# Kernel tuning notes

Measured on AMD Instinct MI355X. Metric: run time of the kernel, lower is better.

The kernel has to match this reference:

```python
import jax, jax.numpy as jnp
from jax import lax
import numpy as np

N, M, P, K = 2, 16384, 5023, 4
C_PLANE, HP = 32, 256
OUT_DIM = 32


def _harmonic(x):
    # pytorch3d HarmonicEmbedding(n=4, logspace, omega_0=1, append_input=True)
    f = jnp.asarray([1.0, 2.0, 4.0, 8.0], x.dtype)
    e = (x[..., None] * f).reshape(x.shape[:-1] + (-1,))  # [..., 12]
    return jnp.concatenate([jnp.sin(e), jnp.cos(e), x], axis=-1)  # [..., 27]


def _grid_sample2d(img, grid):
    # img [C,H,W], grid [M,2] (x->W, y->H) in [-1,1]; bilinear, zero pad, align_corners=False
    C, H, W = img.shape
    x = (grid[:, 0] + 1.0) * (W / 2.0) - 0.5
    y = (grid[:, 1] + 1.0) * (H / 2.0) - 0.5
    x0 = jnp.floor(x); y0 = jnp.floor(y)
    x1 = x0 + 1.0; y1 = y0 + 1.0
    wx1 = x - x0; wx0 = 1.0 - wx1
    wy1 = y - y0; wy0 = 1.0 - wy1
    def gather(ix, iy):
        valid = ((ix >= 0) & (ix < W) & (iy >= 0) & (iy < H)).astype(img.dtype)
        ixc = jnp.clip(ix, 0, W - 1).astype(jnp.int32)
        iyc = jnp.clip(iy, 0, H - 1).astype(jnp.int32)
        return img[:, iyc, ixc] * valid[None, :]  # [C,M]
    out = (gather(x0, y0) * (wx0 * wy0) + gather(x1, y0) * (wx1 * wy0)
           + gather(x0, y1) * (wx0 * wy1) + gather(x1, y1) * (wx1 * wy1))
    return out.T  # [M,C]


def _forward(coordinates, directions, points_position, tex_tplanes, emb_table,
             pw1, pb1, pw2, pb2, fw1, fb1, fw2, fb2, fw3, fb3, dw, db, rw1, rb1, rw2, rb2):
    c = coordinates
    p = points_position
    # --- triplane sampling (EG3D projections (x,y),(x,z),(z,x)), mean over planes ---
    proj = jnp.stack([c[..., :2],
                      c[..., jnp.array([0, 2])],
                      c[..., jnp.array([2, 0])]], axis=1)  # [N,3,M,2]
    tex = jax.vmap(jax.vmap(_grid_sample2d))(tex_tplanes, proj).mean(axis=1)  # [N,M,32]
    # --- KNN (squared distances, ascending, as pytorch3d knn_points) ---
    d2 = (jnp.sum(c * c, -1)[:, :, None] + jnp.sum(p * p, -1)[:, None, :]
          - 2.0 * jnp.einsum('nmc,npc->nmp', c, p))  # [N,M,P]
    negd, idx = lax.top_k(-d2, K)
    dist = -negd  # [N,M,K]
    nn = jax.vmap(lambda pts, i: pts[i])(p, idx)  # [N,M,K,3]
    pf = emb_table[idx]  # [N,M,K,32]
    rel = c[:, :, None, :] - nn
    rel = rel / jnp.maximum(jnp.linalg.norm(rel, axis=-1, keepdims=True), 1e-12)
    h = jnp.concatenate([pf, _harmonic(rel)], axis=-1)  # [N,M,K,59]
    h = jax.nn.relu(h @ pw1 + pb1) @ pw2 + pb2  # [N,M,K,32]
    w = 1.0 / dist
    w = w / jnp.sum(w, axis=1, keepdims=True)  # dim=1 exactly as in source
    pts_feat = jnp.sum(h * w[..., None], axis=2)  # [N,M,32]
    # --- dense MLP stack ---
    feat = jnp.concatenate([tex, pts_feat], axis=-1)  # [N,M,64]
    feat = jax.nn.relu(feat @ fw1 + fb1)
    feat = jax.nn.relu(feat @ fw2 + fb2)
    feat = feat @ fw3 + fb3  # [N,M,128]
    selector = jnp.all((c > -1.0) & (c < 1.0), axis=-1)  # [N,M]
    raw = (jax.nn.softplus(10.0 * (feat @ dw + db)) / 10.0) * selector[..., None]
    densities = 1.0 - jnp.exp(-raw)
    rays = directions / jnp.maximum(jnp.linalg.norm(directions, axis=-1, keepdims=True), 1e-12)
    rgb = jnp.concatenate([feat, _harmonic(rays)], axis=-1)  # [N,M,155]
    rgb = jax.nn.relu(rgb @ rw1 + rb1) @ rw2 + rb2  # [N,M,OUT_DIM]
    rgb = jnp.concatenate([jax.nn.sigmoid(rgb[..., :3]) * (1.0 + 2 * 0.001) - 0.001,
                           rgb[..., 3:]], axis=-1)
    return densities, rgb, dist


def setup_inputs() -> dict:
    key = jax.random.key(0)
    ks = jax.random.split(key, 16)
    rn = lambda k, s, sc=1.0: jax.random.normal(k, s, jnp.float32) * sc
    def lin(k, i, o):
        k1, k2 = jax.random.split(k)
        return rn(k1, (i, o), 1.0 / np.sqrt(i)), rn(k2, (o,), 0.01)
    coordinates = jax.random.uniform(ks[0], (N, M, 3), jnp.float32)
    directions = rn(ks[1], (N, M, 3))
    points_position = jax.random.uniform(ks[2], (N, P, 3), jnp.float32)
    tex_tplanes = rn(ks[3], (N, 3, C_PLANE, HP, HP))
    emb_table = rn(ks[4], (P, 32), 0.02)
    pw1, pb1 = lin(ks[5], 32 + 27, 64)
    pw2, pb2 = lin(ks[6], 64, 32)
    fw1, fb1 = lin(ks[7], 64, 128)
    fw2, fb2 = lin(ks[8], 128, 128)
    fw3, fb3 = lin(ks[9], 128, 128)
    dw, db = lin(ks[10], 128, 1)
    rw1, rb1 = lin(ks[11], 128 + 27, 64)
    rw2, rb2 = lin(ks[12], 64, OUT_DIM)
    return dict(coordinates=coordinates, directions=directions, points_position=points_position,
                tex_tplanes=tex_tplanes, emb_table=emb_table, pw1=pw1, pb1=pb1, pw2=pw2, pb2=pb2,
                fw1=fw1, fb1=fb1, fw2=fw2, fb2=fb2, fw3=fw3, fb3=fb3, dw=dw, db=db,
                rw1=rw1, rb1=rb1, rw2=rw2, rb2=rb2)


def reference(coordinates, directions, points_position, tex_tplanes, emb_table,
              pw1, pb1, pw2, pb2, fw1, fb1, fw2, fb2, fw3, fb3, dw, db, rw1, rb1, rw2, rb2):
    return _forward(coordinates, directions, points_position, tex_tplanes, emb_table,
                    pw1, pb1, pw2, pb2, fw1, fb1, fw2, fb2, fw3, fb3, dw, db, rw1, rb1, rw2, rb2)
```

## Files before the change

kernel.cpp:

```cpp
#include <hip/hip_runtime.h>
#include <float.h>
#include <math.h>

#define NB 2
#define MQ 16384
#define NQ (NB*MQ)
#define PP 5023
#define KNN 4
#define HPX 256
#define HWSZ (HPX*HPX)
#define GD 12
#define GC (GD*GD*GD)
#define CAND_MAX 1024

#define OUT_RGB_OFF  ((size_t)NQ)
#define OUT_DIST_OFF ((size_t)NQ + (size_t)NQ*32)

#define WS_SUMS_OFF   ((size_t)0x80000)
#define WS_PCNT_OFF   ((size_t)0x81000)
#define WS_PSTART_OFF ((size_t)0x85000)
#define WS_PCUR_OFF   ((size_t)0x89000)
#define WS_QCNT_OFF   ((size_t)0x8D000)
#define WS_QSTART_OFF ((size_t)0x91000)
#define WS_QCUR_OFF   ((size_t)0x95000)
#define WS_QID_OFF    ((size_t)0x99000)
#define WS_PG_OFF     ((size_t)0xC0000)
#define WS_PID_OFF    ((size_t)0xF0000)
#define WS_WP_OFF     ((size_t)0x100000)
#define WS_TEX_OFF    ((size_t)0x120000)

#define WP_PW1 0
#define WP_PW2 1920
#define WP_FW1 2944
#define WP_FW2 7040
#define WP_FW3 15232
#define WP_DW  23424
#define WP_RW1 23488
#define WP_RW2 28480

typedef __attribute__((ext_vector_type(2))) _Float16 half2v;

static __device__ __forceinline__ unsigned int pk2(float a, float b) {
    half2v h; h[0] = (_Float16)a; h[1] = (_Float16)b;
    return __builtin_bit_cast(unsigned int, h);
}
static __device__ __forceinline__ float2 upk(unsigned int u) {
    half2v h = __builtin_bit_cast(half2v, u);
    return make_float2((float)h[0], (float)h[1]);
}
static __device__ __forceinline__ float dot2(unsigned int a, unsigned int b, float c) {
    return __builtin_amdgcn_fdot2(__builtin_bit_cast(half2v, a),
                                  __builtin_bit_cast(half2v, b), c, false);
}
static __device__ __forceinline__ int cell_of(float x) {
    int g = (int)(x * (float)GD);
    return (g < 0) ? 0 : ((g > GD-1) ? GD-1 : g);
}

struct FusedArgs {
    const float* src[8];
    int off[8]; int din[8]; int dout[8];
};
__global__ __launch_bounds__(256) void k_fused(
    FusedArgs a, unsigned int* __restrict__ wp,
    const float* __restrict__ tex, unsigned int* __restrict__ tex16,
    const float* __restrict__ pts, const float* __restrict__ coords,
    unsigned int* __restrict__ pcnt, unsigned int* __restrict__ qcnt,
    int use_t)
{
    const int b = blockIdx.x;
    const int tid = threadIdx.x;
    if (b < 1536) {
        if (!use_t) return;
        const int n3 = b >> 8;
        const int hw = ((b & 255) << 8) + tid;
        const float* s = tex + (size_t)n3 * 32 * HWSZ + hw;
        float v[32];
#pragma unroll
        for (int c = 0; c < 32; ++c) v[c] = s[(size_t)c * HWSZ];
        uint4* d = (uint4*)(tex16 + ((size_t)n3 * HWSZ + hw) * 16);
#pragma unroll
        for (int c = 0; c < 4; ++c)
            d[c] = make_uint4(pk2(v[8*c], v[8*c+1]), pk2(v[8*c+2], v[8*c+3]),
                              pk2(v[8*c+4], v[8*c+5]), pk2(v[8*c+6], v[8*c+7]));
    } else if (b < 1536 + 256) {
        const int b2 = b - 1536;
        const int mid = b2 >> 5;
        const int idx = (b2 & 31) * 256 + tid;
        const int DIN = a.din[mid], DOUT = a.dout[mid];
        const int din2 = (DIN + 1) >> 1;
        if (idx >= din2 * DOUT) return;
        const int i2 = idx / DOUT, j = idx - i2 * DOUT;
        const float* s = a.src[mid];
        const float lo = s[(2*i2) * DOUT + j];
        const float hi = (2*i2 + 1 < DIN) ? s[(2*i2 + 1) * DOUT + j] : 0.f;
        wp[a.off[mid] + idx] = pk2(lo, hi);
    } else {
        const int i = (b - 1792) * 256 + tid;
        if (i < NB * PP) {
            const int n = (i >= PP) ? 1 : 0;
            const float px = pts[3*i], py = pts[3*i+1], pz = pts[3*i+2];
            const int c = (cell_of(pz)*GD + cell_of(py))*GD + cell_of(px);
            atomicAdd(&pcnt[n*GC + c], 1u);
        } else if (i - NB*PP < NQ) {
            const int q = i - NB*PP;
            const int n = q >> 14;
            const float cx = coords[3*q], cy = coords[3*q+1], cz = coords[3*q+2];
            const int c = (cell_of(cz)*GD + cell_of(cy))*GD + cell_of(cx);
            atomicAdd(&qcnt[n*GC + c], 1u);
        }
    }
}

__global__ __launch_bounds__(1024) void k_scan2(const unsigned int* __restrict__ pcnt,
                                                unsigned int* __restrict__ psta,
                                                unsigned int* __restrict__ pcur,
                                                const unsigned int* __restrict__ qcnt,
                                                unsigned int* __restrict__ qsta,
                                                unsigned int* __restrict__ qcur) {
    __shared__ unsigned int sc[1024];
    const int t = threadIdx.x;
#pragma unroll 1
    for (int which = 0; which < 2; ++which) {
        const unsigned int* cnt = which ? qcnt : pcnt;
        unsigned int* start  = which ? qsta : psta;
        unsigned int* cursor = which ? qcur : pcur;
        const int stride = which ? MQ : PP;
#pragma unroll 1
        for (int n = 0; n < 2; ++n) {
            const unsigned int* c = cnt + n*GC;
            unsigned int a = (2*t   < GC) ? c[2*t]   : 0u;
            unsigned int b = (2*t+1 < GC) ? c[2*t+1] : 0u;
            unsigned int s = a + b;
            sc[t] = s;
            __syncthreads();
            for (int off = 1; off < 1024; off <<= 1) {
                unsigned int v = (t >= off) ? sc[t - off] : 0u;
                __syncthreads();
                sc[t] += v;
                __syncthreads();
            }
            unsigned int excl = sc[t] - s;
            unsigned int base = n * stride;
            if (2*t < GC)   { start[n*GC + 2*t]   = base + excl;
                              cursor[n*GC + 2*t]  = base + excl; }
            if (2*t+1 < GC) { start[n*GC + 2*t+1] = base + excl + a;
                              cursor[n*GC + 2*t+1]= base + excl + a; }
            __syncthreads();
        }
    }
}

__global__ __launch_bounds__(256) void k_scatter(const float* __restrict__ pts,
                                                 const float* __restrict__ coords,
                                                 unsigned int* __restrict__ pcur,
                                                 unsigned int* __restrict__ qcur,
                                                 float4* __restrict__ pg,
                                                 int* __restrict__ pid,
                                                 int* __restrict__ qid) {
    const int i = blockIdx.x * 256 + threadIdx.x;
    if (i < NB * PP) {
        const int n = (i >= PP) ? 1 : 0;
        const int local = i - n * PP;
        const float px = pts[3*i], py = pts[3*i+1], pz = pts[3*i+2];
        const int c = (cell_of(pz)*GD + cell_of(py))*GD + cell_of(px);
        const unsigned int pos = atomicAdd(&pcur[n*GC + c], 1u);
        pg[pos] = make_float4(px, py, pz, fmaf(px, px, fmaf(py, py, pz*pz)));
        pid[pos] = local;
    } else if (i - NB*PP < NQ) {
        const int q = i - NB*PP;
        const int n = q >> 14;
        const float cx = coords[3*q], cy = coords[3*q+1], cz = coords[3*q+2];
        const int c = (cell_of(cz)*GD + cell_of(cy))*GD + cell_of(cx);
        const unsigned int pos = atomicAdd(&qcur[n*GC + c], 1u);
        qid[pos] = q;
    }
}

__global__ __launch_bounds__(256) void k_knn_cell(
    const float* __restrict__ coords,
    const unsigned int* __restrict__ pstart, const unsigned int* __restrict__ pcnt,
    const float4* __restrict__ pg, const int* __restrict__ pid,
    const unsigned int* __restrict__ qstart, const unsigned int* __restrict__ qcnt,
    const int* __restrict__ qid,
    float* __restrict__ odist, int* __restrict__ oidx)
{
    __shared__ float4 cand[CAND_MAX];
    __shared__ int    cidx[CAND_MAX];
    __shared__ unsigned int rs[25], ro[26];
    const int tid = threadIdx.x;
    const int bid = blockIdx.x;
    const int n = bid / GC, c = bid % GC;
    const unsigned int qn = qcnt[n*GC + c];
    if (qn == 0) return;
    const int gz = c / (GD*GD), gy = (c / GD) % GD, gx = c % GD;

    const int x0 = max(gx-2,0), x1 = min(gx+2,GD-1);
    const int y0 = max(gy-2,0), y1 = min(gy+2,GD-1), ny = y1-y0+1;
    const int z0 = max(gz-2,0), z1 = min(gz+2,GD-1), nz = z1-z0+1;
    const int nrow = ny*nz;

    __shared__ unsigned int rcnt[25];
    if (tid < nrow) {
        const int yy = y0 + tid % ny;
        const int zz = z0 + tid / ny;
        const int c0 = n*GC + (zz*GD + yy)*GD + x0;
        const int c1 = n*GC + (zz*GD + yy)*GD + x1;
        const unsigned int s = pstart[c0];
        rs[tid]   = s;
        rcnt[tid] = (pstart[c1] + pcnt[c1]) - s;
    }
    __syncthreads();
    if (tid == 0) {
        unsigned int acc = 0; ro[0] = 0;
        for (int t = 0; t < nrow; ++t) { acc += rcnt[t]; ro[t+1] = acc; }
    }
    __syncthreads();
    const unsigned int total = ro[nrow];
    const bool ovf = (total > CAND_MAX);
    if (!ovf) {
        for (unsigned int i = tid; i < total; i += 256) {
            int lo = 0, hi = nrow;
            while (hi - lo > 1) { int mid = (lo + hi) >> 1; if (ro[mid] <= i) lo = mid; else hi = mid; }
            const unsigned int src = rs[lo] + (i - ro[lo]);
            cand[i] = pg[src];
            cidx[i] = pid[src];
        }
    }
    __syncthreads();

    const float w = 1.0f / (float)GD;
    const float thresh = 4.f * w * w * 0.999f;
    const int grp = tid >> 4, l16 = tid & 15;
    const unsigned int qs = qstart[n*GC + c];

#define INS4(d, i) { \
        bool L3 = ((d) < bd3) || ((d) == bd3 && (i) < bi3); \
        bool L2 = ((d) < bd2) || ((d) == bd2 && (i) < bi2); \
        bool L1 = ((d) < bd1) || ((d) == bd1 && (i) < bi1); \
        bool L0 = ((d) < bd0) || ((d) == bd0 && (i) < bi0); \
        bd3 = L3 ? (L2 ? bd2 : (d)) : bd3;  bi3 = L3 ? (L2 ? bi2 : (i)) : bi3; \
        bd2 = L2 ? (L1 ? bd1 : (d)) : bd2;  bi2 = L2 ? (L1 ? bi1 : (i)) : bi2; \
        bd1 = L1 ? (L0 ? bd0 : (d)) : bd1;  bi1 = L1 ? (L0 ? bi0 : (i)) : bi1; \
        bd0 = L0 ? (d) : bd0;               bi0 = L0 ? (i) : bi0; }

#define MERGE16() { \
        float bd[4] = { bd0, bd1, bd2, bd3 }; \
        int   bi[4] = { bi0, bi1, bi2, bi3 }; \
        for (int mask = 1; mask < 16; mask <<= 1) { \
            float od[4]; int oi[4]; \
            for (int j = 0; j < 4; ++j) { od[j] = __shfl_xor(bd[j], mask); \
                                          oi[j] = __shfl_xor(bi[j], mask); } \
            float e[4]; int ei[4]; \
            for (int j = 0; j < 4; ++j) { \
                float ad = bd[j], xd = od[3-j]; \
                int   ai = bi[j], xi = oi[3-j]; \
                bool ta = (ad < xd) || (ad == xd && ai < xi); \
                e[j] = ta ? ad : xd; ei[j] = ta ? ai : xi; \
            } \
            { bool sw = (e[2] < e[0]) || (e[2] == e[0] && ei[2] < ei[0]); \
              if (sw) { float td=e[0]; e[0]=e[2]; e[2]=td; int ti=ei[0]; ei[0]=ei[2]; ei[2]=ti; } } \
            { bool sw = (e[3] < e[1]) || (e[3] == e[1] && ei[3] < ei[1]); \
              if (sw) { float td=e[1]; e[1]=e[3]; e[3]=td; int ti=ei[1]; ei[1]=ei[3]; ei[3]=ti; } } \
            { bool sw = (e[1] < e[0]) || (e[1] == e[0] && ei[1] < ei[0]); \
              if (sw) { float td=e[0]; e[0]=e[1]; e[1]=td; int ti=ei[0]; ei[0]=ei[1]; ei[1]=ti; } } \
            { bool sw = (e[3] < e[2]) || (e[3] == e[2] && ei[3] < ei[2]); \
              if (sw) { float td=e[2]; e[2]=e[3]; e[3]=td; int ti=ei[2]; ei[2]=ei[3]; ei[3]=ti; } } \
            for (int j = 0; j < 4; ++j) { bd[j] = e[j]; bi[j] = ei[j]; } \
        } \
        bd0 = bd[0]; bd1 = bd[1]; bd2 = bd[2]; bd3 = bd[3]; \
        bi0 = bi[0]; bi1 = bi[1]; bi2 = bi[2]; bi3 = bi[3]; }

#pragma unroll 1
    for (unsigned int qb = 0; qb < qn; qb += 16) {
        const unsigned int qi = qb + grp;
        if (qi >= qn) continue;
        const int q = qid[qs + qi];
        const float cx = coords[3*q], cy = coords[3*q+1], cz = coords[3*q+2];
        const float ccq = fmaf(cx, cx, fmaf(cy, cy, cz*cz));

        float bd0 = FLT_MAX, bd1 = FLT_MAX, bd2 = FLT_MAX, bd3 = FLT_MAX;
        int   bi0 = 0x7fffffff, bi1 = 0x7fffffff, bi2 = 0x7fffffff, bi3 = 0x7fffffff;

        if (!ovf) {
#pragma unroll 1
            for (unsigned int j = l16; j < total; j += 16) {
                const float4 P = cand[j];
                const int i = cidx[j];
                const float dt = fmaf(cx, P.x, fmaf(cy, P.y, cz * P.z));
                const float d = fmaf(-2.0f, dt, ccq + P.w);
                INS4(d, i)
            }
            MERGE16()
        }
        if (ovf || !(bd3 < thresh)) {
            bd0 = bd1 = bd2 = bd3 = FLT_MAX;
            bi0 = bi1 = bi2 = bi3 = 0x7fffffff;
#pragma unroll 1
            for (int j = l16; j < PP; j += 16) {
                const float4 P = pg[n*PP + j];
                const int i = pid[n*PP + j];
                const float dt = fmaf(cx, P.x, fmaf(cy, P.y, cz * P.z));
                const float d = fmaf(-2.0f, dt, ccq + P.w);
                INS4(d, i)
            }
            MERGE16()
        }
        if (l16 == 0) {
            *(float4*)(odist + (size_t)q*4) = make_float4(bd0, bd1, bd2, bd3);
            *(int4*)(oidx + (size_t)q*4)    = make_int4(bi0, bi1, bi2, bi3);
        }
    }
#undef INS4
#undef MERGE16
}

__global__ __launch_bounds__(1024) void k_sums(const float* __restrict__ dist,
                                               float* __restrict__ sums) {
    const int b = blockIdx.x;
    const int n = b >> 2, k = b & 3;
    float s = 0.f;
    for (int m = threadIdx.x; m < MQ; m += 1024)
        s += 1.0f / dist[((size_t)n * MQ + m) * 4 + k];
    __shared__ float red[1024];
    red[threadIdx.x] = s;
    __syncthreads();
    for (int off = 512; off > 0; off >>= 1) {
        if (threadIdx.x < off) red[threadIdx.x] += red[threadIdx.x + off];
        __syncthreads();
    }
    if (threadIdx.x == 0) sums[b] = red[0];
}

static __device__ __forceinline__ float harm_val(int h, float rx, float ry, float rz) {
    if (h >= 27) return 0.f;
    float v;
    if (h < 24) {
        int base = (h < 12) ? h : (h - 12);
        float rv = (base >> 2) == 0 ? rx : ((base >> 2) == 1 ? ry : rz);
        float e = rv * (float)(1 << (base & 3));
        v = (h < 12) ? sinf(e) : cosf(e);
    } else {
        v = (h == 24) ? rx : ((h == 25) ? ry : rz);
    }
    return v;
}

#define SW 128

template<int DIN2, int DOUT, int TILE>
__device__ __forceinline__ void gemv2(const unsigned int* Xp, int lane,
                                      const unsigned int* Wl,
                                      const float* __restrict__ bias, int j0,
                                      float (&aa)[TILE], float (&ab)[TILE]) {
    static_assert(TILE % 4 == 0, "");
#pragma unroll
    for (int u = 0; u < TILE; ++u) { aa[u] = bias[j0 + u]; ab[u] = aa[u]; }
#pragma unroll
    for (int i2 = 0; i2 < DIN2; ++i2) {
        const uint2 xv = *(const uint2*)(Xp + i2 * SW + 2*lane);
        const uint4* wr = (const uint4*)(Wl + i2 * DOUT + j0);
#pragma unroll
        for (int t = 0; t < TILE/4; ++t) {
            const uint4 w4 = wr[t];
            aa[4*t+0] = dot2(xv.x, w4.x, aa[4*t+0]);  ab[4*t+0] = dot2(xv.y, w4.x, ab[4*t+0]);
            aa[4*t+1] = dot2(xv.x, w4.y, aa[4*t+1]);  ab[4*t+1] = dot2(xv.y, w4.y, ab[4*t+1]);
            aa[4*t+2] = dot2(xv.x, w4.z, aa[4*t+2]);  ab[4*t+2] = dot2(xv.y, w4.z, ab[4*t+2]);
            aa[4*t+3] = dot2(xv.x, w4.w, aa[4*t+3]);  ab[4*t+3] = dot2(xv.y, w4.w, ab[4*t+3]);
        }
    }
}

__global__ __launch_bounds__(1024, 1) void k_main(
    const float* __restrict__ coords, const float* __restrict__ dirs,
    const float* __restrict__ pts, const float* __restrict__ tex_raw,
    const unsigned int* __restrict__ tex16, const float* __restrict__ emb,
    const unsigned int* __restrict__ wp,
    const float* __restrict__ pb1, const float* __restrict__ pb2,
    const float* __restrict__ fb1, const float* __restrict__ fb2,
    const float* __restrict__ fb3, const float* __restrict__ db,
    const float* __restrict__ rb1, const float* __restrict__ rb2,
    const int* __restrict__ idxbuf, const float* __restrict__ distbuf,
    const float* __restrict__ sums, float* __restrict__ out, int use_tex_t)
{
    __shared__ unsigned int S[128 * SW];
    __shared__ __align__(16) unsigned int W[8192];
    __shared__ float Rstg[128 * 33];
    const int tid  = threadIdx.x;
    const int lane = tid & 63;
    const int wv   = __builtin_amdgcn_readfirstlane(tid >> 6);
    const int q0   = blockIdx.x * 128;
    const int n    = q0 >> 14;
    const int qa   = q0 + 2*lane;

#define STAGE(dstu4, srcoff, len) { \
        const uint4* s4_ = (const uint4*)(wp + (srcoff)); \
        for (int i_ = tid; i_ < (len)/4; i_ += 1024) ((uint4*)W)[(dstu4) + i_] = s4_[i_]; }

    auto gatherA = [&](int kk) {
#pragma unroll
        for (int s = 0; s < 2; ++s) {
            const int q = qa + s;
            const int id = idxbuf[(size_t)q*4 + kk];
            if (wv < 8) {
                const float4 e = *(const float4*)(emb + (size_t)id * 32 + wv*4);
                S[(64 + 2*wv    )*SW + 2*lane + s] = pk2(e.x, e.y);
                S[(64 + 2*wv + 1)*SW + 2*lane + s] = pk2(e.z, e.w);
            } else {
                const int w8 = wv - 8;
                if (w8 < 7) {
                    const float cx = coords[q*3+0], cy = coords[q*3+1], cz = coords[q*3+2];
                    const float nx = pts[((size_t)n*PP + id)*3 + 0];
                    const float ny = pts[((size_t)n*PP + id)*3 + 1];
                    const float nz = pts[((size_t)n*PP + id)*3 + 2];
                    float rx = cx - nx, ry = cy - ny, rz = cz - nz;
                    float nrm = sqrtf(fmaf(rx, rx, fmaf(ry, ry, rz*rz)));
                    float inv = 1.f / fmaxf(nrm, 1e-12f);
                    rx *= inv; ry *= inv; rz *= inv;
#pragma unroll
                    for (int t = 0; t < 2; ++t) {
                        const int pr = 2*w8 + t;
                        S[(80 + pr)*SW + 2*lane + s] =
                            pk2(harm_val(2*pr, rx, ry, rz), harm_val(2*pr + 1, rx, ry, rz));
                    }
                }
            }
        }
    };

    unsigned int tex_pack[2];
    {
        const int g = wv;
#pragma unroll
        for (int s = 0; s < 2; ++s) {
            const int q = qa + s;
            const float cx = coords[q*3+0], cy = coords[q*3+1], cz = coords[q*3+2];
            float a0 = 0.f, a1 = 0.f;
#pragma unroll
            for (int pl = 0; pl < 3; ++pl) {
                float gx = (pl == 2) ? cz : cx;
                float gy = (pl == 0) ? cy : ((pl == 1) ? cz : cx);
                float x = (gx + 1.f) * 128.f - 0.5f;
                float y = (gy + 1.f) * 128.f - 0.5f;
                float x0f = floorf(x), y0f = floorf(y);
                float wx1 = x - x0f, wy1 = y - y0f;
                float wx0 = 1.f - wx1, wy0 = 1.f - wy1;
                int x0 = (int)x0f, y0 = (int)y0f;
                int n3 = n * 3 + pl;
                int  xs[4] = { x0, x0+1, x0,   x0+1 };
                int  ys[4] = { y0, y0,   y0+1, y0+1 };
                float wt[4] = { wx0*wy0, wx1*wy0, wx0*wy1, wx1*wy1 };
#pragma unroll
                for (int c = 0; c < 4; ++c) {
                    int xi = xs[c], yi = ys[c];
                    if (xi >= 0 && xi < HPX && yi >= 0 && yi < HPX) {
                        float wgt = wt[c];
                        if (use_tex_t) {
                            const unsigned int v = tex16[
                                ((size_t)n3 * HWSZ + (size_t)yi * HPX + xi) * 16 + g];
                            const float2 f = upk(v);
                            a0 = fmaf(wgt, f.x, a0);
                            a1 = fmaf(wgt, f.y, a1);
                        } else {
                            size_t base = ((size_t)(n3 * 32 + g * 2)) * HWSZ + (size_t)yi * HPX + xi;
                            a0 = fmaf(wgt, tex_raw[base], a0);
                            a1 = fmaf(wgt, tex_raw[base + HWSZ], a1);
                        }
                    }
                }
            }
            tex_pack[s] = pk2(a0 * (1.f/3.f), a1 * (1.f/3.f));
        }
    }

    STAGE(0, WP_PW1, 1920)
    STAGE(512, WP_PW2, 1024)
    gatherA(0);
    __syncthreads();

#pragma unroll 1
    for (int k = 0; k < KNN; ++k) {
        {
            float aa[4], ab[4];
            gemv2<30, 64, 4>(S + 64*SW, lane, W, pb1, wv * 4, aa, ab);
            S[(96 + 2*wv    )*SW + 2*lane + 0] = pk2(fmaxf(aa[0], 0.f), fmaxf(aa[1], 0.f));
            S[(96 + 2*wv    )*SW + 2*lane + 1] = pk2(fmaxf(ab[0], 0.f), fmaxf(ab[1], 0.f));
            S[(96 + 2*wv + 1)*SW + 2*lane + 0] = pk2(fmaxf(aa[2], 0.f), fmaxf(aa[3], 0.f));
            S[(96 + 2*wv + 1)*SW + 2*lane + 1] = pk2(fmaxf(ab[2], 0.f), fmaxf(ab[3], 0.f));
        }
        __syncthreads();
        {
            float aa[2], ab[2];
            aa[0] = pb2[wv*2 + 0]; aa[1] = pb2[wv*2 + 1];
            ab[0] = aa[0]; ab[1] = aa[1];
#pragma unroll
            for (int i2 = 0; i2 < 32; ++i2) {
                const uint2 xv = *(const uint2*)(S + (96 + i2)*SW + 2*lane);
                const unsigned int w0 = W[2048 + i2*32 + wv*2 + 0];
                const unsigned int w1 = W[2048 + i2*32 + wv*2 + 1];
                aa[0] = dot2(xv.x, w0, aa[0]);  ab[0] = dot2(xv.y, w0, ab[0]);
                aa[1] = dot2(xv.x, w1, aa[1]);  ab[1] = dot2(xv.y, w1, ab[1]);
            }
            const float da  = distbuf[(size_t)qa*4 + k];
            const float dbq = distbuf[(size_t)(qa+1)*4 + k];
            const float wka = (1.0f / da)  / sums[n*4 + k];
            const float wkb = (1.0f / dbq) / sums[n*4 + k];
            S[(k*16 + wv)*SW + 2*lane + 0] = pk2(wka * aa[0], wka * aa[1]);
            S[(k*16 + wv)*SW + 2*lane + 1] = pk2(wkb * ab[0], wkb * ab[1]);
        }
        if (k < KNN-1) gatherA(k+1);
        __syncthreads();
    }

    {
        S[(64 + wv)*SW + 2*lane + 0] = tex_pack[0];
        S[(64 + wv)*SW + 2*lane + 1] = tex_pack[1];
#pragma unroll
        for (int s = 0; s < 2; ++s) {
            float a = 0.f, b = 0.f;
#pragma unroll
            for (int k = 0; k < 4; ++k) {
                float2 v = upk(S[(k*16 + wv)*SW + 2*lane + s]);
                a += v.x; b += v.y;
            }
            S[(80 + wv)*SW + 2*lane + s] = pk2(a, b);
        }
    }
    STAGE(0, WP_FW1, 4096)
    __syncthreads();
    {
        float aa[8], ab[8];
        gemv2<32, 128, 8>(S + 64*SW, lane, W, fb1, wv * 8, aa, ab);
#pragma unroll
        for (int u = 0; u < 4; ++u) {
            S[(4*wv + u)*SW + 2*lane + 0] = pk2(fmaxf(aa[2*u], 0.f), fmaxf(aa[2*u+1], 0.f));
            S[(4*wv + u)*SW + 2*lane + 1] = pk2(fmaxf(ab[2*u], 0.f), fmaxf(ab[2*u+1], 0.f));
        }
    }
    __syncthreads();
    STAGE(0, WP_FW2, 8192)
    __syncthreads();
    {
        float aa[8], ab[8];
        gemv2<64, 128, 8>(S, lane, W, fb2, wv * 8, aa, ab);
#pragma unroll
        for (int u = 0; u < 4; ++u) {
            S[(64 + 4*wv + u)*SW + 2*lane + 0] = pk2(fmaxf(aa[2*u], 0.f), fmaxf(aa[2*u+1], 0.f));
            S[(64 + 4*wv + u)*SW + 2*lane + 1] = pk2(fmaxf(ab[2*u], 0.f), fmaxf(ab[2*u+1], 0.f));
        }
    }
    __syncthreads();
    STAGE(0, WP_FW3, 8192)
    __syncthreads();
    {
        float aa[8], ab[8];
        gemv2<64, 128, 8>(S + 64*SW, lane, W, fb3, wv * 8, aa, ab);
#pragma unroll
        for (int u = 0; u < 4; ++u) {
            S[(4*wv + u)*SW + 2*lane + 0] = pk2(aa[2*u], aa[2*u+1]);
            S[(4*wv + u)*SW + 2*lane + 1] = pk2(ab[2*u], ab[2*u+1]);
        }
    }
    __syncthreads();
    STAGE(0, WP_RW1, 4992)
    STAGE(1248, WP_RW2, 1024)
    STAGE(1504, WP_DW, 64)
    if (wv < 14) {
#pragma unroll
        for (int s = 0; s < 2; ++s) {
            const int q = qa + s;
            float dx = dirs[q*3+0], dy = dirs[q*3+1], dz = dirs[q*3+2];
            float dn = sqrtf(fmaf(dx, dx, fmaf(dy, dy, dz*dz)));
            float inv = 1.f / fmaxf(dn, 1e-12f);
            dx *= inv; dy *= inv; dz *= inv;
            S[(64 + wv)*SW + 2*lane + s] = pk2(harm_val(2*wv, dx, dy, dz),
                                               harm_val(2*wv + 1, dx, dy, dz));
        }
    }
    __syncthreads();
    {
        float aa[4], ab[4];
        gemv2<78, 64, 4>(S, lane, W, rb1, wv * 4, aa, ab);
        S[(78 + 2*wv    )*SW + 2*lane + 0] = pk2(fmaxf(aa[0], 0.f), fmaxf(aa[1], 0.f));
        S[(78 + 2*wv    )*SW + 2*lane + 1] = pk2(fmaxf(ab[0], 0.f), fmaxf(ab[1], 0.f));
        S[(78 + 2*wv + 1)*SW + 2*lane + 0] = pk2(fmaxf(aa[2], 0.f), fmaxf(aa[3], 0.f));
        S[(78 + 2*wv + 1)*SW + 2*lane + 1] = pk2(fmaxf(ab[2], 0.f), fmaxf(ab[3], 0.f));
    }
    __syncthreads();
    {
        float aa[2], ab[2];
        aa[0] = rb2[wv*2 + 0]; aa[1] = rb2[wv*2 + 1];
        ab[0] = aa[0]; ab[1] = aa[1];
#pragma unroll
        for (int i2 = 0; i2 < 32; ++i2) {
            const uint2 xv = *(const uint2*)(S + (78 + i2)*SW + 2*lane);
            const unsigned int w0 = W[4992 + i2*32 + wv*2 + 0];
            const unsigned int w1 = W[4992 + i2*32 + wv*2 + 1];
            aa[0] = dot2(xv.x, w0, aa[0]);  ab[0] = dot2(xv.y, w0, ab[0]);
            aa[1] = dot2(xv.x, w1, aa[1]);  ab[1] = dot2(xv.y, w1, ab[1]);
        }
#pragma unroll
        for (int u = 0; u < 2; ++u) {
            const int j = wv*2 + u;
            float va = (u == 0) ? aa[0] : aa[1];
            float vb = (u == 0) ? ab[0] : ab[1];
            if (j < 3) {
                va = 1.002f * (1.f / (1.f + expf(-va))) - 0.001f;
                vb = 1.002f * (1.f / (1.f + expf(-vb))) - 0.001f;
            }
            Rstg[(2*lane    ) * 33 + j] = va;
            Rstg[(2*lane + 1) * 33 + j] = vb;
        }
        if (wv == 15) {
            float za = db[0], zb = db[0];
#pragma unroll 8
            for (int i2 = 0; i2 < 64; ++i2) {
                const uint2 xv = *(const uint2*)(S + i2*SW + 2*lane);
                const unsigned int wz = W[6016 + i2];
                za = dot2(xv.x, wz, za);
                zb = dot2(xv.y, wz, zb);
            }
#pragma unroll
            for (int s = 0; s < 2; ++s) {
                const int q = qa + s;
                const float z = (s == 0) ? za : zb;
                const float cx = coords[q*3+0], cy = coords[q*3+1], cz = coords[q*3+2];
                float selv = (cx > -1.f && cx < 1.f && cy > -1.f && cy < 1.f &&
                              cz > -1.f && cz < 1.f) ? 1.f : 0.f;
                float t10 = 10.f * z;
                float sp = (t10 > 20.f) ? t10 : log1pf(expf(t10));
                float raw = sp * 0.1f * selv;
                out[q] = 1.f - expf(-raw);
            }
        }
    }
    __syncthreads();
    {
        const int cq = tid >> 3;
        const int j0 = (tid & 7) * 4;
        float4 v;
        v.x = Rstg[cq*33 + j0 + 0];
        v.y = Rstg[cq*33 + j0 + 1];
        v.z = Rstg[cq*33 + j0 + 2];
        v.w = Rstg[cq*33 + j0 + 3];
        *(float4*)(out + OUT_RGB_OFF + ((size_t)(q0 + cq))*32 + j0) = v;
    }
#undef STAGE
}

extern "C" void kernel_launch(void* const* d_in, const int* in_sizes, int n_in,
                              void* d_out, int out_size, void* d_ws, size_t ws_size,
                              hipStream_t stream) {
    (void)in_sizes; (void)n_in; (void)out_size;
    const float* coords = (const float*)d_in[0];
    const float* dirs   = (const float*)d_in[1];
    const float* pts    = (const float*)d_in[2];
    const float* tex    = (const float*)d_in[3];
    const float* emb    = (const float*)d_in[4];
    const float* pw1 = (const float*)d_in[5];  const float* pb1 = (const float*)d_in[6];
    const float* pw2 = (const float*)d_in[7];  const float* pb2 = (const float*)d_in[8];
    const float* fw1 = (const float*)d_in[9];  const float* fb1 = (const float*)d_in[10];
    const float* fw2 = (const float*)d_in[11]; const float* fb2 = (const float*)d_in[12];
    const float* fw3 = (const float*)d_in[13]; const float* fb3 = (const float*)d_in[14];
    const float* dw  = (const float*)d_in[15]; const float* db  = (const float*)d_in[16];
    const float* rw1 = (const float*)d_in[17]; const float* rb1 = (const float*)d_in[18];
    const float* rw2 = (const float*)d_in[19]; const float* rb2 = (const float*)d_in[20];

    float*        out     = (float*)d_out;
    int*          wsidx   = (int*)d_ws;
    float*        wssums  = (float*)((char*)d_ws + WS_SUMS_OFF);
    unsigned int* wspcnt  = (unsigned int*)((char*)d_ws + WS_PCNT_OFF);
    unsigned int* wspsta  = (unsigned int*)((char*)d_ws + WS_PSTART_OFF);
    unsigned int* wspcur  = (unsigned int*)((char*)d_ws + WS_PCUR_OFF);
    unsigned int* wsqcnt  = (unsigned int*)((char*)d_ws + WS_QCNT_OFF);
    unsigned int* wsqsta  = (unsigned int*)((char*)d_ws + WS_QSTART_OFF);
    unsigned int* wsqcur  = (unsigned int*)((char*)d_ws + WS_QCUR_OFF);
    int*          wsqid   = (int*)((char*)d_ws + WS_QID_OFF);
    float4*       wspg    = (float4*)((char*)d_ws + WS_PG_OFF);
    int*          wspid   = (int*)((char*)d_ws + WS_PID_OFF);
    unsigned int* wswp    = (unsigned int*)((char*)d_ws + WS_WP_OFF);
    unsigned int* wstex   = (unsigned int*)((char*)d_ws + WS_TEX_OFF);

    const size_t need_tex = WS_TEX_OFF + (size_t)6 * HWSZ * 16 * 4;
    const int use_t = (ws_size >= need_tex) ? 1 : 0;

    FusedArgs fa;
    fa.src[0] = pw1; fa.off[0] = WP_PW1; fa.din[0] = 59;  fa.dout[0] = 64;
    fa.src[1] = pw2; fa.off[1] = WP_PW2; fa.din[1] = 64;  fa.dout[1] = 32;
    fa.src[2] = fw1; fa.off[2] = WP_FW1; fa.din[2] = 64;  fa.dout[2] = 128;
    fa.src[3] = fw2; fa.off[3] = WP_FW2; fa.din[3] = 128; fa.dout[3] = 128;
    fa.src[4] = fw3; fa.off[4] = WP_FW3; fa.din[4] = 128; fa.dout[4] = 128;
    fa.src[5] = dw;  fa.off[5] = WP_DW;  fa.din[5] = 128; fa.dout[5] = 1;
    fa.src[6] = rw1; fa.off[6] = WP_RW1; fa.din[6] = 155; fa.dout[6] = 64;
    fa.src[7] = rw2; fa.off[7] = WP_RW2; fa.din[7] = 64;  fa.dout[7] = 32;

    const int nitems = NB*PP + NQ;
    const int count_blocks = (nitems + 255) / 256;
    hipMemsetAsync((char*)d_ws + WS_PCNT_OFF, 0, WS_QSTART_OFF - WS_PCNT_OFF, stream);
    k_fused<<<1792 + count_blocks, 256, 0, stream>>>(fa, wswp, tex, wstex,
                                                     pts, coords, wspcnt, wsqcnt, use_t);
    k_scan2<<<1, 1024, 0, stream>>>(wspcnt, wspsta, wspcur, wsqcnt, wsqsta, wsqcur);
    k_scatter<<<count_blocks, 256, 0, stream>>>(pts, coords, wspcur, wsqcur,
                                                wspg, wspid, wsqid);
    k_knn_cell<<<NB*GC, 256, 0, stream>>>(coords, wspsta, wspcnt, wspg, wspid,
                                          wsqsta, wsqcnt, wsqid,
                                          out + OUT_DIST_OFF, wsidx);
    k_sums<<<8, 1024, 0, stream>>>(out + OUT_DIST_OFF, wssums);
    k_main<<<NQ / 128, 1024, 0, stream>>>(coords, dirs, pts, tex, wstex, emb,
                                          wswp, pb1, pb2, fb1, fb2, fb3, db, rb1, rb2,
                                          wsidx, out + OUT_DIST_OFF, wssums, out, use_t);
}
```

Before: 272.0 us.

## Double-buffer MLP weights in LDS and accumulate KNN features in registers

New measurement: 321.8 us. +18.3%, slower.

```diff
diff --git a/kernel.cpp b/kernel.cpp
--- a/kernel.cpp
+++ b/kernel.cpp
@@ -384,8 +384,8 @@
     const float* __restrict__ sums, float* __restrict__ out, int use_tex_t)
 {
     __shared__ unsigned int S[128 * SW];
-    __shared__ __align__(16) unsigned int W[8192];
-    __shared__ float Rstg[128 * 33];
+    __shared__ __align__(16) unsigned int W[16384];
+    __shared__ __align__(16) float Rstg[128 * 33];
     const int tid  = threadIdx.x;
     const int lane = tid & 63;
     const int wv   = __builtin_amdgcn_readfirstlane(tid >> 6);
@@ -473,11 +473,13 @@
         }
     }
 
-    STAGE(0, WP_PW1, 1920)
-    STAGE(512, WP_PW2, 1024)
+    STAGE(0,    WP_PW1, 1920)
+    STAGE(512,  WP_PW2, 1024)
+    STAGE(1024, WP_FW1, 4096)
     gatherA(0);
     __syncthreads();
 
+    float fA0 = 0.f, fA1 = 0.f, fB0 = 0.f, fB1 = 0.f;
 #pragma unroll 1
     for (int k = 0; k < KNN; ++k) {
         {
@@ -488,6 +490,7 @@
             S[(96 + 2*wv + 1)*SW + 2*lane + 0] = pk2(fmaxf(aa[2], 0.f), fmaxf(aa[3], 0.f));
             S[(96 + 2*wv + 1)*SW + 2*lane + 1] = pk2(fmaxf(ab[2], 0.f), fmaxf(ab[3], 0.f));
         }
+        if (k == 0) STAGE(2048, WP_FW2, 8192)
         __syncthreads();
         {
             float aa[2], ab[2];
@@ -505,32 +508,23 @@
             const float dbq = distbuf[(size_t)(qa+1)*4 + k];
             const float wka = (1.0f / da)  / sums[n*4 + k];
             const float wkb = (1.0f / dbq) / sums[n*4 + k];
-            S[(k*16 + wv)*SW + 2*lane + 0] = pk2(wka * aa[0], wka * aa[1]);
-            S[(k*16 + wv)*SW + 2*lane + 1] = pk2(wkb * ab[0], wkb * ab[1]);
-        }
-        if (k < KNN-1) gatherA(k+1);
+            fA0 = fmaf(wka, aa[0], fA0);  fA1 = fmaf(wka, aa[1], fA1);
+            fB0 = fmaf(wkb, ab[0], fB0);  fB1 = fmaf(wkb, ab[1], fB1);
+        }
+        if (k < KNN-1) {
+            gatherA(k+1);
+        } else {
+            S[(64 + wv)*SW + 2*lane + 0] = tex_pack[0];
+            S[(64 + wv)*SW + 2*lane + 1] = tex_pack[1];
+            S[(80 + wv)*SW + 2*lane + 0] = pk2(fA0, fA1);
+            S[(80 + wv)*SW + 2*lane + 1] = pk2(fB0, fB1);
+        }
         __syncthreads();
     }
 
-    {
-        S[(64 + wv)*SW + 2*lane + 0] = tex_pack[0];
-        S[(64 + wv)*SW + 2*lane + 1] = tex_pack[1];
-#pragma unroll
-        for (int s = 0; s < 2; ++s) {
-            float a = 0.f, b = 0.f;
-#pragma unroll
-            for (int k = 0; k < 4; ++k) {
-                float2 v = upk(S[(k*16 + wv)*SW + 2*lane + s]);
-                a += v.x; b += v.y;
-            }
-            S[(80 + wv)*SW + 2*lane + s] = pk2(a, b);
-        }
-    }
-    STAGE(0, WP_FW1, 4096)
-    __syncthreads();
     {
         float aa[8], ab[8];
-        gemv2<32, 128, 8>(S + 64*SW, lane, W, fb1, wv * 8, aa, ab);
+        gemv2<32, 128, 8>(S + 64*SW, lane, W + 4096, fb1, wv * 8, aa, ab);
 #pragma unroll
         for (int u = 0; u < 4; ++u) {
             S[(4*wv + u)*SW + 2*lane + 0] = pk2(fmaxf(aa[2*u], 0.f), fmaxf(aa[2*u+1], 0.f));
@@ -538,34 +532,18 @@
         }
     }
     __syncthreads();
-    STAGE(0, WP_FW2, 8192)
-    __syncthreads();
     {
         float aa[8], ab[8];
-        gemv2<64, 128, 8>(S, lane, W, fb2, wv * 8, aa, ab);
+        gemv2<64, 128, 8>(S, lane, W + 8192, fb2, wv * 8, aa, ab);
 #pragma unroll
         for (int u = 0; u < 4; ++u) {
             S[(64 + 4*wv + u)*SW + 2*lane + 0] = pk2(fmaxf(aa[2*u], 0.f), fmaxf(aa[2*u+1], 0.f));
             S[(64 + 4*wv + u)*SW + 2*lane + 1] = pk2(fmaxf(ab[2*u], 0.f), fmaxf(ab[2*u+1], 0.f));
         }
     }
-    __syncthreads();
     STAGE(0, WP_FW3, 8192)
-    __syncthreads();
-    {
-        float aa[8], ab[8];
-        gemv2<64, 128, 8>(S + 64*SW, lane, W, fb3, wv * 8, aa, ab);
-#pragma unroll
-        for (int u = 0; u < 4; ++u) {
-            S[(4*wv + u)*SW + 2*lane + 0] = pk2(aa[2*u], aa[2*u+1]);
-            S[(4*wv + u)*SW + 2*lane + 1] = pk2(ab[2*u], ab[2*u+1]);
-        }
-    }
-    __syncthreads();
-    STAGE(0, WP_RW1, 4992)
-    STAGE(1248, WP_RW2, 1024)
-    STAGE(1504, WP_DW, 64)
     if (wv < 14) {
+        unsigned int* uR = (unsigned int*)Rstg;
 #pragma unroll
         for (int s = 0; s < 2; ++s) {
             const int q = qa + s;
@@ -573,14 +551,40 @@
             float dn = sqrtf(fmaf(dx, dx, fmaf(dy, dy, dz*dz)));
             float inv = 1.f / fmaxf(dn, 1e-12f);
             dx *= inv; dy *= inv; dz *= inv;
-            S[(64 + wv)*SW + 2*lane + s] = pk2(harm_val(2*wv, dx, dy, dz),
-                                               harm_val(2*wv + 1, dx, dy, dz));
-        }
-    }
+            uR[wv*128 + 2*lane + s] = pk2(harm_val(2*wv, dx, dy, dz),
+                                          harm_val(2*wv + 1, dx, dy, dz));
+        }
+    }
+    __syncthreads();
+    {
+        float aa[8], ab[8];
+        gemv2<64, 128, 8>(S + 64*SW, lane, W, fb3, wv * 8, aa, ab);
+#pragma unroll
+        for (int u = 0; u < 4; ++u) {
+            S[(4*wv + u)*SW + 2*lane + 0] = pk2(aa[2*u], aa[2*u+1]);
+            S[(4*wv + u)*SW + 2*lane + 1] = pk2(ab[2*u], ab[2*u+1]);
+        }
+    }
+    STAGE(2048, WP_RW1, 4992)
+    STAGE(3296, WP_RW2, 1024)
+    STAGE(3552, WP_DW, 64)
     __syncthreads();
     {
         float aa[4], ab[4];
-        gemv2<78, 64, 4>(S, lane, W, rb1, wv * 4, aa, ab);
+#pragma unroll
+        for (int u = 0; u < 4; ++u) { aa[u] = rb1[wv*4 + u]; ab[u] = aa[u]; }
+        const unsigned int* uR = (const unsigned int*)Rstg;
+#pragma unroll
+        for (int i2 = 0; i2 < 78; ++i2) {
+            const uint2 xv = (i2 < 64)
+                ? *(const uint2*)(S + i2 * SW + 2*lane)
+                : *(const uint2*)(uR + (i2 - 64) * 128 + 2*lane);
+            const uint4 w4 = *(const uint4*)(W + 8192 + i2*64 + wv*4);
+            aa[0] = dot2(xv.x, w4.x, aa[0]);  ab[0] = dot2(xv.y, w4.x, ab[0]);
+            aa[1] = dot2(xv.x, w4.y, aa[1]);  ab[1] = dot2(xv.y, w4.y, ab[1]);
+            aa[2] = dot2(xv.x, w4.z, aa[2]);  ab[2] = dot2(xv.y, w4.z, ab[2]);
+            aa[3] = dot2(xv.x, w4.w, aa[3]);  ab[3] = dot2(xv.y, w4.w, ab[3]);
+        }
         S[(78 + 2*wv    )*SW + 2*lane + 0] = pk2(fmaxf(aa[0], 0.f), fmaxf(aa[1], 0.f));
         S[(78 + 2*wv    )*SW + 2*lane + 1] = pk2(fmaxf(ab[0], 0.f), fmaxf(ab[1], 0.f));
         S[(78 + 2*wv + 1)*SW + 2*lane + 0] = pk2(fmaxf(aa[2], 0.f), fmaxf(aa[3], 0.f));
@@ -594,8 +598,8 @@
 #pragma unroll
         for (int i2 = 0; i2 < 32; ++i2) {
             const uint2 xv = *(const uint2*)(S + (78 + i2)*SW + 2*lane);
-            const unsigned int w0 = W[4992 + i2*32 + wv*2 + 0];
-            const unsigned int w1 = W[4992 + i2*32 + wv*2 + 1];
+            const unsigned int w0 = W[13184 + i2*32 + wv*2 + 0];
+            const unsigned int w1 = W[13184 + i2*32 + wv*2 + 1];
             aa[0] = dot2(xv.x, w0, aa[0]);  ab[0] = dot2(xv.y, w0, ab[0]);
             aa[1] = dot2(xv.x, w1, aa[1]);  ab[1] = dot2(xv.y, w1, ab[1]);
         }
@@ -616,7 +620,7 @@
 #pragma unroll 8
             for (int i2 = 0; i2 < 64; ++i2) {
                 const uint2 xv = *(const uint2*)(S + i2*SW + 2*lane);
-                const unsigned int wz = W[6016 + i2];
+                const unsigned int wz = W[14208 + i2];
                 za = dot2(xv.x, wz, za);
                 zb = dot2(xv.y, wz, zb);
             }
```
